# Performance work log

Hardware: AMD Instinct MI355X
Metric: run time of the kernel (lower is better)

The kernel has to match this reference:

```python
import jax, jax.numpy as jnp
import numpy as np

D = 256          # input_dim == layer_size
L = 2            # n_hidden_layers in ResLinear
B, S = 8, 4096
LR = 1e-3        # AdamW learning_rate
WD = 1e-2        # weight_decay
MAX_ALR = 0.1    # max adaptive lr
EPS = 1e-8       # AdamW eps


def _lmm(Ws, bs, x):
    # ResLinear: residual MLP blocks, hidden size D.
    # Ws: [L, D, D], bs: [L, D], x: [..., D]
    for i in range(L):
        x = x + jax.nn.silu(x @ Ws[i] + bs[i])
    return x


def setup_inputs() -> dict:
    key = jax.random.key(0)
    ks = jax.random.split(key, 9)
    scale = 0.05
    return {
        "x": jax.random.normal(ks[0], (B, S, D), dtype=jnp.float32),
        "Wk": jax.random.normal(ks[1], (D, D), dtype=jnp.float32) * scale,
        "Wq": jax.random.normal(ks[2], (D, D), dtype=jnp.float32) * scale,
        "Wv": jax.random.normal(ks[3], (D, D), dtype=jnp.float32) * scale,
        "Wlr": jax.random.normal(ks[4], (D, 1), dtype=jnp.float32) * scale,
        "blr": jnp.zeros((1,), dtype=jnp.float32),
        "Ws": jax.random.normal(ks[5], (L, D, D), dtype=jnp.float32) * scale,
        "bs": jnp.zeros((L, D), dtype=jnp.float32),
    }


def reference(x, Wk, Wq, Wv, Wlr, blr, Ws, bs):
    # Projections (LinearProjection: bias-free D->D linear)
    keys = x @ Wk          # [B, S, D]
    queries = x @ Wq       # [B, S, D]
    values = x @ Wv        # [B, S, D]
    # AdaptiveLR: sigmoid gate scaled to max_adaptive_lr, one scalar per token
    alr = (jax.nn.sigmoid(x @ Wlr + blr) * MAX_ALR).reshape(-1)  # [B*S]

    def loss_fn(params):
        Ws_, bs_ = params
        preds = _lmm(Ws_, bs_, keys).reshape(-1, D)
        tgt = values.reshape(-1, D)
        per_tok = jnp.mean((preds - tgt) ** 2, axis=-1)  # [B*S]
        return jnp.sum(per_tok * alr)

    gWs, gbs = jax.grad(loss_fn)((Ws, bs))

    # Single AdamW step from zero optimizer state (step=1):
    #   m_hat = g, v_hat = g^2  ->  p' = p*(1 - lr*wd) - lr * g / (|g| + eps)
    def adamw_step(p, g):
        return p * (1.0 - LR * WD) - LR * g / (jnp.sqrt(g * g) + EPS)

    nWs = adamw_step(Ws, gWs)
    nbs = adamw_step(bs, gbs)

    retrieved = _lmm(nWs, nbs, queries)  # [B, S, D]
    # surprises = -grads
    return retrieved, -gWs, -gbs
```

## Files before the change

### kernel.cpp

```cpp
#include <hip/hip_runtime.h>
#include <math.h>


#define NTOK 32768
#define NM ((size_t)NTOK * 256)
#define LRc 1e-3f
#define WDc 1e-2f
#define EPSc 1e-8f

typedef __attribute__((ext_vector_type(8))) short bf16x8;
typedef __attribute__((ext_vector_type(4))) float f32x4;

__device__ __forceinline__ float b2f(unsigned short u) {
    union { unsigned int i; float f; } c;
    c.i = ((unsigned int)u) << 16;
    return c.f;
}
__device__ __forceinline__ unsigned short f2b(float f) {
    union { float f; unsigned int i; } c;
    c.f = f;
    unsigned int i = c.i;
    return (unsigned short)((i + 0x7FFFu + ((i >> 16) & 1u)) >> 16);
}
__device__ __forceinline__ float sigm(float z) { return 1.f / (1.f + __expf(-z)); }
__device__ __forceinline__ float siluf(float z) { return z * sigm(z); }
__device__ __forceinline__ float dsiluf(float z) {
    float s = sigm(z);
    return s * (1.f + z * (1.f - s));
}
__device__ __forceinline__ void unpack4(uint2 u, float* f) {
    f[0] = b2f(u.x & 0xFFFF); f[1] = b2f(u.x >> 16);
    f[2] = b2f(u.y & 0xFFFF); f[3] = b2f(u.y >> 16);
}
__device__ __forceinline__ uint2 pack4(const float* f) {
    uint2 o;
    o.x = (unsigned)f2b(f[0]) | ((unsigned)f2b(f[1]) << 16);
    o.y = (unsigned)f2b(f[2]) | ((unsigned)f2b(f[3]) << 16);
    return o;
}

#define WSTR 264
#define SSTR 40

template <int EPI>
__global__ __launch_bounds__(512, 4) void wgemm_k(
    const unsigned short* __restrict__ A, const unsigned short* __restrict__ Bt,
    const float* __restrict__ bias, const unsigned short* __restrict__ Rin,
    const unsigned short* __restrict__ Zin, const unsigned short* __restrict__ Vb,
    const float* __restrict__ alr, unsigned short* __restrict__ Cb,
    float* __restrict__ Cf, unsigned short* __restrict__ Zout,
    unsigned short* __restrict__ Rout, size_t zcs) {
    __shared__ unsigned short Ws[128 * WSTR];
    __shared__ unsigned short Sc[8][16 * SSTR];
    Bt += (size_t)blockIdx.z * 65536;
    Cb += (size_t)blockIdx.z * zcs;
    const int n0 = blockIdx.x * 128, m0 = blockIdx.y * 128;
    const int tid = threadIdx.x, lane = tid & 63, wv = tid >> 6;
    const int cc = lane & 15, q = lane >> 4;

    const int t0 = m0 + wv * 16;
    const unsigned short* xp = A + (size_t)(t0 + cc) * 256 + q * 8;
    bf16x8 xf[8];
#pragma unroll
    for (int c = 0; c < 8; c++) xf[c] = *(const bf16x8*)(xp + c * 32);

#pragma unroll
    for (int it = 0; it < 8; it++) {
        int i = it * 512 + tid;
        int row = i >> 5, g8 = i & 31;
        *(uint4*)&Ws[row * WSTR + g8 * 8] =
            *(const uint4*)(Bt + (size_t)(n0 + row) * 256 + g8 * 8);
    }
    __syncthreads();

    f32x4 acc[8];
#pragma unroll
    for (int t = 0; t < 8; t++) acc[t] = (f32x4){0.f, 0.f, 0.f, 0.f};

#pragma unroll
    for (int c = 0; c < 8; c++) {
#pragma unroll
        for (int nt = 0; nt < 8; nt++) {
            bf16x8 wf = *(const bf16x8*)&Ws[(nt * 16 + cc) * WSTR + c * 32 + q * 8];
            acc[nt] = __builtin_amdgcn_mfma_f32_16x16x32_bf16(wf, xf[c],
                                                              acc[nt], 0, 0, 0);
        }
    }

    const int tok = t0 + cc;
    float lalr = 0.f;
    if (EPI == 5) lalr = alr[tok] * (2.f / 256.f);
    unsigned short* sc = &Sc[wv][0];
    const int rtok = lane >> 2, roct = (lane & 3) * 8;

#pragma unroll
    for (int pr = 0; pr < 4; pr++) {
        float o2[2][4], z2[2][4];
#pragma unroll
        for (int h = 0; h < 2; h++) {
            const int nt = pr * 2 + h;
            const int gcol = n0 + nt * 16 + q * 4;
            const size_t off = (size_t)tok * 256 + gcol;
            f32x4 c = acc[nt];
            float v[4] = {c[0], c[1], c[2], c[3]};
            if (EPI == 0) {
#pragma unroll
                for (int r = 0; r < 4; r++) o2[h][r] = v[r];
            } else if (EPI == 1) {
                float bv[4], a[4];
                *(float4*)bv = *(const float4*)(bias + gcol);
                unpack4(*(const uint2*)(A + off), a);
#pragma unroll
                for (int r = 0; r < 4; r++) {
                    float z = v[r] + bv[r];
                    z2[h][r] = z;
                    o2[h][r] = a[r] + siluf(z);
                }
            } else if (EPI == 5) {
                float bv[4], a[4], vv[4];
                *(float4*)bv = *(const float4*)(bias + gcol);
                unpack4(*(const uint2*)(A + off), a);
                unpack4(*(const uint2*)(Vb + off), vv);
#pragma unroll
                for (int r = 0; r < 4; r++) {
                    float z = v[r] + bv[r];
                    float h2 = a[r] + siluf(z);
                    float dh = lalr * (h2 - vv[r]);
                    o2[h][r] = dh * dsiluf(z);
                    z2[h][r] = dh;
                }
            } else if (EPI == 2) {
                float ri[4], zi[4];
                unpack4(*(const uint2*)(Rin + off), ri);
                unpack4(*(const uint2*)(Zin + off), zi);
#pragma unroll
                for (int r = 0; r < 4; r++)
                    o2[h][r] = (v[r] + ri[r]) * dsiluf(zi[r]);
            } else {
                float bv[4], a[4];
                *(float4*)bv = *(const float4*)(bias + gcol);
                unpack4(*(const uint2*)(A + off), a);
#pragma unroll
                for (int r = 0; r < 4; r++) o2[h][r] = a[r] + siluf(v[r] + bv[r]);
            }
            if (EPI == 4) {
                *(float4*)(Cf + off) = *(float4*)o2[h];
            }
        }
        if (EPI == 4) continue;
#pragma unroll
        for (int h = 0; h < 2; h++)
            *(uint2*)&sc[cc * SSTR + h * 16 + q * 4] = pack4(o2[h]);
        uint4 pk = *(const uint4*)&sc[rtok * SSTR + roct];
        *(uint4*)(Cb + (size_t)(t0 + rtok) * 256 + n0 + pr * 32 + roct) = pk;
        if (EPI == 1 || EPI == 5) {
#pragma unroll
            for (int h = 0; h < 2; h++)
                *(uint2*)&sc[cc * SSTR + h * 16 + q * 4] = pack4(z2[h]);
            uint4 pk2 = *(const uint4*)&sc[rtok * SSTR + roct];
            unsigned short* P2 = (EPI == 1) ? Zout : Rout;
            *(uint4*)(P2 + (size_t)(t0 + rtok) * 256 + n0 + pr * 32 + roct) = pk2;
        }
    }
}

__global__ __launch_bounds__(256, 2) void rgemm_k(
    const unsigned short* __restrict__ Kb, const unsigned short* __restrict__ h1b,
    const unsigned short* __restrict__ dz0b,
    const unsigned short* __restrict__ dz1b, float* __restrict__ pbuf) {
    __shared__ unsigned short As[128 * 40];
    __shared__ unsigned short Bs2[128 * 40];
    const int z = blockIdx.z, layer = z >> 6, zc = z & 63;
    const unsigned short* Ag = layer ? h1b : Kb;
    const unsigned short* Bg = layer ? dz1b : dz0b;
    const int t0 = zc * 512;
    const int j0 = blockIdx.x * 128, i0 = blockIdx.y * 128;
    const int tid = threadIdx.x, lane = tid & 63, wave = tid >> 6;
    const int wr = (wave >> 1) * 64, wc = (wave & 1) * 64;
    const int fr = lane & 15, fk = (lane >> 4) * 8;
    const int pt = (tid >> 4) * 2, pi = (tid & 15) * 8;

    f32x4 acc[4][4];
#pragma unroll
    for (int i = 0; i < 4; i++)
#pragma unroll
        for (int j = 0; j < 4; j++) acc[i][j] = (f32x4){0.f, 0.f, 0.f, 0.f};

    for (int tt = t0; tt < t0 + 512; tt += 32) {
        uint4 a0 = *(const uint4*)(Ag + (size_t)(tt + pt) * 256 + i0 + pi);
        uint4 a1 = *(const uint4*)(Ag + (size_t)(tt + pt + 1) * 256 + i0 + pi);
        uint4 b0 = *(const uint4*)(Bg + (size_t)(tt + pt) * 256 + j0 + pi);
        uint4 b1 = *(const uint4*)(Bg + (size_t)(tt + pt + 1) * 256 + j0 + pi);
        const unsigned int* aw0 = (const unsigned int*)&a0;
        const unsigned int* aw1 = (const unsigned int*)&a1;
        const unsigned int* bw0 = (const unsigned int*)&b0;
        const unsigned int* bw1 = (const unsigned int*)&b1;
#pragma unroll
        for (int ii = 0; ii < 8; ii++) {
            unsigned int alo = (aw0[ii >> 1] >> (16 * (ii & 1))) & 0xFFFFu;
            unsigned int ahi = (aw1[ii >> 1] >> (16 * (ii & 1))) & 0xFFFFu;
            unsigned int blo = (bw0[ii >> 1] >> (16 * (ii & 1))) & 0xFFFFu;
            unsigned int bhi = (bw1[ii >> 1] >> (16 * (ii & 1))) & 0xFFFFu;
            const int ad = ((pi + ii) * 40 + pt) >> 1;
            ((unsigned int*)As)[ad] = alo | (ahi << 16);
            ((unsigned int*)Bs2)[ad] = blo | (bhi << 16);
        }
        __syncthreads();
        bf16x8 af[4], bfr[4];
#pragma unroll
        for (int i = 0; i < 4; i++) {
            af[i] = *(const bf16x8*)&As[(wr + i * 16 + fr) * 40 + fk];
            bfr[i] = *(const bf16x8*)&Bs2[(wc + i * 16 + fr) * 40 + fk];
        }
#pragma unroll
        for (int i = 0; i < 4; i++)
#pragma unroll
            for (int j = 0; j < 4; j++)
                acc[i][j] = __builtin_amdgcn_mfma_f32_16x16x32_bf16(
                    af[i], bfr[j], acc[i][j], 0, 0, 0);
        __syncthreads();
    }

    float* P = pbuf + (size_t)((layer << 6) + zc) * 65536;
    const int r0 = (lane >> 4) * 4, cc = lane & 15;
#pragma unroll
    for (int mi = 0; mi < 4; mi++)
#pragma unroll
        for (int ni = 0; ni < 4; ni++) {
            f32x4 c = acc[mi][ni];
#pragma unroll
            for (int r = 0; r < 4; r++)
                P[(size_t)(i0 + wr + mi * 16 + r0 + r) * 256 +
                  (j0 + wc + ni * 16 + cc)] = c[r];
        }
}

__global__ void reduce_k(const float* __restrict__ pbuf, float* __restrict__ accW) {
    int idx = blockIdx.x * 256 + threadIdx.x;
    int layer = idx >> 16, rc = idx & 65535;
    const float* p = pbuf + (size_t)layer * 64 * 65536 + rc;
    float s = 0.f;
#pragma unroll 8
    for (int c = 0; c < 64; c++) s += p[(size_t)c * 65536];
    accW[idx] = s;
}

__global__ __launch_bounds__(256) void colsum_k(const unsigned short* __restrict__ dz,
                                                float* __restrict__ gb) {
    const int col = threadIdx.x;
    const size_t r0 = (size_t)blockIdx.x * 128;
    float s0 = 0, s1 = 0, s2 = 0, s3 = 0;
    for (int r = 0; r < 128; r += 4) {
        s0 += b2f(dz[(r0 + r) * 256 + col]);
        s1 += b2f(dz[(r0 + r + 1) * 256 + col]);
        s2 += b2f(dz[(r0 + r + 2) * 256 + col]);
        s3 += b2f(dz[(r0 + r + 3) * 256 + col]);
    }
    atomicAdd(&gb[col], s0 + s1 + s2 + s3);
}

__global__ __launch_bounds__(256) void prep_k(const float* __restrict__ x,
                                              const float* __restrict__ Wlr,
                                              const float* __restrict__ blr,
                                              unsigned short* __restrict__ xb,
                                              float* __restrict__ alr) {
    const int wave = threadIdx.x >> 6, lane = threadIdx.x & 63;
    const int r = blockIdx.x * 4 + wave;
    float4 w = *(const float4*)(Wlr + lane * 4);
    float4 v = *(const float4*)(x + (size_t)r * 256 + lane * 4);
    float s = v.x * w.x + v.y * w.y + v.z * w.z + v.w * w.w;
    unsigned int p0 = (unsigned int)f2b(v.x) | ((unsigned int)f2b(v.y) << 16);
    unsigned int p1 = (unsigned int)f2b(v.z) | ((unsigned int)f2b(v.w) << 16);
    *(uint2*)(xb + (size_t)r * 256 + lane * 4) = make_uint2(p0, p1);
#pragma unroll
    for (int off = 32; off; off >>= 1) s += __shfl_down(s, off);
    if (lane == 0) alr[r] = 0.1f * sigm(s + blr[0]);
}

__global__ void wprep_k(const float* __restrict__ Wk, const float* __restrict__ Wq,
                        const float* __restrict__ Wv, const float* __restrict__ Ws,
                        unsigned short* __restrict__ wt) {
    const int z = blockIdx.y;
    const int idx = blockIdx.x * 256 + threadIdx.x;
    const float* src = z == 0 ? Wk : z == 1 ? Wq : z == 2 ? Wv
                     : z == 3 ? Ws : Ws + 65536;
    unsigned short* dst = wt + (size_t)z * 65536;
    float v = src[idx];
    if (z == 5)
        dst[idx] = f2b(v);
    else
        dst[(idx & 255) * 256 + (idx >> 8)] = f2b(v);
}

__global__ void adamw_w_k(const float* __restrict__ Ws,
                          const float* __restrict__ accW,
                          unsigned short* __restrict__ nWt,
                          float* __restrict__ outSW) {
    int idx = blockIdx.x * 256 + threadIdx.x;
    float g = accW[idx];
    outSW[idx] = -g;
    float nw = Ws[idx] * (1.f - LRc * WDc) - LRc * g / (fabsf(g) + EPSc);
    int l = idx >> 16, k = (idx >> 8) & 255, n = idx & 255;
    nWt[(size_t)l * 65536 + n * 256 + k] = f2b(nw);
}

__global__ void adamw_b_k(const float* __restrict__ bs,
                          const float* __restrict__ accB,
                          float* __restrict__ nb, float* __restrict__ outSb) {
    int idx = blockIdx.x * 256 + threadIdx.x;
    float g = accB[idx];
    outSb[idx] = -g;
    nb[idx] = bs[idx] * (1.f - LRc * WDc) - LRc * g / (fabsf(g) + EPSc);
}

__global__ void zero_k(float* p, int n) {
    int i = blockIdx.x * 256 + threadIdx.x;
    if (i < n) p[i] = 0.f;
}

extern "C" void kernel_launch(void* const* d_in, const int* in_sizes, int n_in,
                              void* d_out, int out_size, void* d_ws,
                              size_t ws_size, hipStream_t stream) {
    const float* x = (const float*)d_in[0];
    const float* Wk = (const float*)d_in[1];
    const float* Wq = (const float*)d_in[2];
    const float* Wv = (const float*)d_in[3];
    const float* Wlr = (const float*)d_in[4];
    const float* blr = (const float*)d_in[5];
    const float* Ws = (const float*)d_in[6];
    const float* bs = (const float*)d_in[7];

    unsigned short* S = (unsigned short*)d_ws;
    unsigned short* xb = S + 0 * NM;
    unsigned short* Kb = S + 1 * NM;
    unsigned short* Qb = S + 2 * NM;
    unsigned short* Vb = S + 3 * NM;
    unsigned short* z0b = S + 4 * NM;
    unsigned short* h1b = S + 5 * NM;
    unsigned short* dz1b = S + 6 * NM;
    unsigned short* dh2b = S + 7 * NM;
    unsigned short* dz0b = S + 8 * NM;
    float* pbuf = (float*)(S + 9 * NM);
    unsigned short* r1b = xb;

    unsigned short* wt = S + 11 * NM;
    unsigned short* W0t = wt + 3 * 65536;
    unsigned short* W1t = wt + 4 * 65536;
    unsigned short* W1b = wt + 5 * 65536;
    unsigned short* nW0t = wt + 6 * 65536;
    unsigned short* nW1t = wt + 7 * 65536;
    float* ft = (float*)(wt + 8 * 65536);
    float* alr = ft;
    float* accW = ft + 32768;
    float* accB = accW + 131072;
    float* nb = accB + 512;

    float* out_ret = (float*)d_out;
    float* out_sW = out_ret + NM;
    float* out_sb = out_sW + 131072;

    dim3 blk5(512);
    dim3 blk(256);
    dim3 g_tall(2, 256);

    zero_k<<<2, blk, 0, stream>>>(accB, 512);
    prep_k<<<8192, blk, 0, stream>>>(x, Wlr, blr, xb, alr);
    wprep_k<<<dim3(256, 6), blk, 0, stream>>>(Wk, Wq, Wv, Ws, wt);

    wgemm_k<0><<<dim3(2, 256, 3), blk5, 0, stream>>>(
        xb, wt, nullptr, nullptr, nullptr, nullptr, nullptr, Kb, nullptr,
        nullptr, nullptr, NM);

    wgemm_k<1><<<g_tall, blk5, 0, stream>>>(Kb, W0t, bs, nullptr, nullptr,
                                            nullptr, nullptr, h1b, nullptr,
                                            z0b, nullptr, 0);

    wgemm_k<5><<<g_tall, blk5, 0, stream>>>(h1b, W1t, bs + 256, nullptr,
                                            nullptr, Vb, alr, dz1b, nullptr,
                                            nullptr, dh2b, 0);
    colsum_k<<<256, blk, 0, stream>>>(dz1b, accB + 256);

    wgemm_k<2><<<g_tall, blk5, 0, stream>>>(dz1b, W1b, nullptr, dh2b, z0b,
                                            nullptr, nullptr, dz0b, nullptr,
                                            nullptr, nullptr, 0);
    colsum_k<<<256, blk, 0, stream>>>(dz0b, accB);

    rgemm_k<<<dim3(2, 2, 128), blk, 0, stream>>>(Kb, h1b, dz0b, dz1b, pbuf);
    reduce_k<<<512, blk, 0, stream>>>(pbuf, accW);

    adamw_w_k<<<512, blk, 0, stream>>>(Ws, accW, nW0t, out_sW);
    adamw_b_k<<<2, blk, 0, stream>>>(bs, accB, nb, out_sb);

    wgemm_k<3><<<g_tall, blk5, 0, stream>>>(Qb, nW0t, nb, nullptr, nullptr,
                                            nullptr, nullptr, r1b, nullptr,
                                            nullptr, nullptr, 0);
    wgemm_k<4><<<g_tall, blk5, 0, stream>>>(r1b, nW1t, nb + 256, nullptr,
                                            nullptr, nullptr, nullptr, nullptr,
                                            out_ret, nullptr, nullptr, 0);
}
```

Before: 286.2 us.

## Restructure weight-gradient GEMM: 512 threads, swizzled LDS, register prefetch

The weight-gradient GEMM kernel now runs with 512 threads per block, split into two halves: one half loads the A operand tile and the other loads the B operand tile. Each thread transposes its loaded data into LDS using an XOR-swizzled layout instead of a padded stride, which is meant to cut LDS bank conflicts. The next chunk of global data is prefetched into registers while the MFMAs run on the current one. Eight waves each compute a 64x32 sub-tile, so each wave holds half as many accumulators; LDS use per block grows and the launch bound claims four blocks per CU.

```diff
diff --git a/kernel.cpp b/kernel.cpp
--- a/kernel.cpp
+++ b/kernel.cpp
@@ -164,74 +164,94 @@
     }
 }
 
-__global__ __launch_bounds__(256, 2) void rgemm_k(
+__global__ __launch_bounds__(512, 4) void rgemm_k(
     const unsigned short* __restrict__ Kb, const unsigned short* __restrict__ h1b,
     const unsigned short* __restrict__ dz0b,
     const unsigned short* __restrict__ dz1b, float* __restrict__ pbuf) {
-    __shared__ unsigned short As[128 * 40];
-    __shared__ unsigned short Bs2[128 * 40];
+    __shared__ unsigned short As[128 * 64];
+    __shared__ unsigned short Bs2[128 * 64];
     const int z = blockIdx.z, layer = z >> 6, zc = z & 63;
     const unsigned short* Ag = layer ? h1b : Kb;
     const unsigned short* Bg = layer ? dz1b : dz0b;
     const int t0 = zc * 512;
     const int j0 = blockIdx.x * 128, i0 = blockIdx.y * 128;
     const int tid = threadIdx.x, lane = tid & 63, wave = tid >> 6;
-    const int wr = (wave >> 1) * 64, wc = (wave & 1) * 64;
-    const int fr = lane & 15, fk = (lane >> 4) * 8;
-    const int pt = (tid >> 4) * 2, pi = (tid & 15) * 8;
-
-    f32x4 acc[4][4];
+
+    const int half = tid >> 8;
+    const int t9 = tid & 255;
+    const int ptq = t9 >> 4;
+    const int pi = (t9 & 15) * 8;
+    const unsigned short* sg = half ? Bg : Ag;
+    const int nb = half ? j0 : i0;
+    unsigned int* dst = (unsigned int*)(half ? Bs2 : As);
+    const unsigned short* gp = sg + (size_t)(t0 + ptq * 2) * 256 + nb + pi;
+
+    const int wr = (wave >> 2) * 64, wc = (wave & 3) * 32;
+    const int fr = lane & 15, fkb = lane >> 4;
+
+    f32x4 acc[4][2];
 #pragma unroll
     for (int i = 0; i < 4; i++)
 #pragma unroll
-        for (int j = 0; j < 4; j++) acc[i][j] = (f32x4){0.f, 0.f, 0.f, 0.f};
-
-    for (int tt = t0; tt < t0 + 512; tt += 32) {
-        uint4 a0 = *(const uint4*)(Ag + (size_t)(tt + pt) * 256 + i0 + pi);
-        uint4 a1 = *(const uint4*)(Ag + (size_t)(tt + pt + 1) * 256 + i0 + pi);
-        uint4 b0 = *(const uint4*)(Bg + (size_t)(tt + pt) * 256 + j0 + pi);
-        uint4 b1 = *(const uint4*)(Bg + (size_t)(tt + pt + 1) * 256 + j0 + pi);
-        const unsigned int* aw0 = (const unsigned int*)&a0;
-        const unsigned int* aw1 = (const unsigned int*)&a1;
-        const unsigned int* bw0 = (const unsigned int*)&b0;
-        const unsigned int* bw1 = (const unsigned int*)&b1;
+        for (int j = 0; j < 2; j++) acc[i][j] = (f32x4){0.f, 0.f, 0.f, 0.f};
+
+    uint4 u0 = *(const uint4*)gp;
+    uint4 u1 = *(const uint4*)(gp + 256);
+    gp += 32 * 256;
+
+    for (int it = 0; it < 16; it++) {
+        const unsigned int* w0 = (const unsigned int*)&u0;
+        const unsigned int* w1 = (const unsigned int*)&u1;
 #pragma unroll
         for (int ii = 0; ii < 8; ii++) {
-            unsigned int alo = (aw0[ii >> 1] >> (16 * (ii & 1))) & 0xFFFFu;
-            unsigned int ahi = (aw1[ii >> 1] >> (16 * (ii & 1))) & 0xFFFFu;
-            unsigned int blo = (bw0[ii >> 1] >> (16 * (ii & 1))) & 0xFFFFu;
-            unsigned int bhi = (bw1[ii >> 1] >> (16 * (ii & 1))) & 0xFFFFu;
-            const int ad = ((pi + ii) * 40 + pt) >> 1;
-            ((unsigned int*)As)[ad] = alo | (ahi << 16);
-            ((unsigned int*)Bs2)[ad] = blo | (bhi << 16);
+            unsigned int lo = (w0[ii >> 1] >> (16 * (ii & 1))) & 0xFFFFu;
+            unsigned int hi = (w1[ii >> 1] >> (16 * (ii & 1))) & 0xFFFFu;
+            const int col = pi + ii;
+            const int s2 = ((col >> 3) ^ col) & 3;
+            const int s4 = ((col >> 2) ^ (col >> 5)) & 1;
+            dst[col * 32 + (ptq ^ (s2 << 2) ^ (s4 << 4))] = lo | (hi << 16);
         }
         __syncthreads();
-        bf16x8 af[4], bfr[4];
+        if (it < 15) {
+            u0 = *(const uint4*)gp;
+            u1 = *(const uint4*)(gp + 256);
+            gp += 32 * 256;
+        }
+        bf16x8 af[4], bfr[2];
 #pragma unroll
         for (int i = 0; i < 4; i++) {
-            af[i] = *(const bf16x8*)&As[(wr + i * 16 + fr) * 40 + fk];
-            bfr[i] = *(const bf16x8*)&Bs2[(wc + i * 16 + fr) * 40 + fk];
+            const int col = wr + i * 16 + fr;
+            const int s2 = ((col >> 3) ^ col) & 3;
+            const int s4 = ((col >> 2) ^ (col >> 5)) & 1;
+            af[i] = *(const bf16x8*)&As[col * 64 + (fkb ^ s2 ^ (s4 << 2)) * 8];
+        }
+#pragma unroll
+        for (int j = 0; j < 2; j++) {
+            const int col = wc + j * 16 + fr;
+            const int s2 = ((col >> 3) ^ col) & 3;
+            const int s4 = ((col >> 2) ^ (col >> 5)) & 1;
+            bfr[j] = *(const bf16x8*)&Bs2[col * 64 + (fkb ^ s2 ^ (s4 << 2)) * 8];
         }
 #pragma unroll
         for (int i = 0; i < 4; i++)
 #pragma unroll
-            for (int j = 0; j < 4; j++)
+            for (int j = 0; j < 2; j++)
                 acc[i][j] = __builtin_amdgcn_mfma_f32_16x16x32_bf16(
                     af[i], bfr[j], acc[i][j], 0, 0, 0);
         __syncthreads();
     }
 
     float* P = pbuf + (size_t)((layer << 6) + zc) * 65536;
-    const int r0 = (lane >> 4) * 4, cc = lane & 15;
+    const int r0 = fkb * 4;
 #pragma unroll
     for (int mi = 0; mi < 4; mi++)
 #pragma unroll
-        for (int ni = 0; ni < 4; ni++) {
+        for (int ni = 0; ni < 2; ni++) {
             f32x4 c = acc[mi][ni];
 #pragma unroll
             for (int r = 0; r < 4; r++)
                 P[(size_t)(i0 + wr + mi * 16 + r0 + r) * 256 +
-                  (j0 + wc + ni * 16 + cc)] = c[r];
+                  (j0 + wc + ni * 16 + fr)] = c[r];
         }
 }
 
@@ -385,7 +405,7 @@
                                             nullptr, nullptr, 0);
     colsum_k<<<256, blk, 0, stream>>>(dz0b, accB);
 
-    rgemm_k<<<dim3(2, 2, 128), blk, 0, stream>>>(Kb, h1b, dz0b, dz1b, pbuf);
+    rgemm_k<<<dim3(2, 2, 128), blk5, 0, stream>>>(Kb, h1b, dz0b, dz1b, pbuf);
     reduce_k<<<512, blk, 0, stream>>>(pbuf, accW);
 
     adamw_w_k<<<512, blk, 0, stream>>>(Ws, accW, nW0t, out_sW);
```

Result: faster. 270.8 us (-5.4%).
